# Performance work log

Measured on AMD Instinct MI355X. Metric: run time of the kernel, lower is better.

Reference implementation:

```python
import jax, jax.numpy as jnp
import numpy as np

D = 1024      # hidden_size
H = 16        # num_heads
HD = D // H   # head_dim = 64
FF = 4096     # intermediate_size
DEPTH = 2
S = 2048      # packed sequence length
NSEG = 4     # number of image segments
EPS = 1e-6


def setup_inputs() -> dict:
    key = jax.random.key(0)
    ks = jax.random.split(key, 8)
    hidden_states = jax.random.normal(ks[0], (S, D), jnp.float32)
    cu_seqlens = jnp.arange(NSEG + 1, dtype=jnp.int32) * (S // NSEG)
    # rotary embedding like RiceRotaryEmbedding(head_dim//2): freqs of dim HD//4
    # per spatial axis, h/w concatenated -> HD//2, then duplicated -> HD
    inv_freq = 1.0 / (10000.0 ** (jnp.arange(0, HD // 2, 2, dtype=jnp.float32) / (HD // 2)))
    pos = jnp.arange(S, dtype=jnp.float32)
    freqs = jnp.outer(pos, inv_freq)                       # [S, HD//4]
    emb = jnp.concatenate([freqs] * 4, axis=-1)            # [S, HD]
    cos, sin = jnp.cos(emb), jnp.sin(emb)

    def w(k, shape, fan):
        return jax.random.normal(k, shape, jnp.float32) / np.sqrt(fan)

    return {
        "hidden_states": hidden_states,
        "cu_seqlens": cu_seqlens,
        "cos": cos,
        "sin": sin,
        "ln1_g": jnp.ones((DEPTH, D), jnp.float32),
        "ln1_b": jnp.zeros((DEPTH, D), jnp.float32),
        "qkv_w": w(ks[1], (DEPTH, D, 3 * D), D),
        "qkv_b": jnp.zeros((DEPTH, 3 * D), jnp.float32),
        "proj_w": w(ks[2], (DEPTH, D, D), D),
        "proj_b": jnp.zeros((DEPTH, D), jnp.float32),
        "ln2_g": jnp.ones((DEPTH, D), jnp.float32),
        "ln2_b": jnp.zeros((DEPTH, D), jnp.float32),
        "fc1_w": w(ks[3], (DEPTH, D, FF), D),
        "fc1_b": jnp.zeros((DEPTH, FF), jnp.float32),
        "fc2_w": w(ks[4], (DEPTH, FF, D), FF),
        "fc2_b": jnp.zeros((DEPTH, D), jnp.float32),
    }


def _ln(x, g, b):
    m = jnp.mean(x, axis=-1, keepdims=True)
    v = jnp.mean(jnp.square(x - m), axis=-1, keepdims=True)
    return (x - m) / jnp.sqrt(v + EPS) * g + b


def _rotate_half(x):
    x1, x2 = jnp.split(x, 2, axis=-1)
    return jnp.concatenate([-x2, x1], axis=-1)


def reference(hidden_states, cu_seqlens, cos, sin,
              ln1_g, ln1_b, qkv_w, qkv_b, proj_w, proj_b,
              ln2_g, ln2_b, fc1_w, fc1_b, fc2_w, fc2_b):
    S_, D_ = hidden_states.shape
    # segment id per token from cu_seqlens -> block-diagonal additive mask
    seg = jnp.searchsorted(cu_seqlens[1:], jnp.arange(S_, dtype=jnp.int32), side="right")
    neg = jnp.finfo(jnp.float32).min
    bias = jnp.where(seg[:, None] == seg[None, :], 0.0, neg)   # [S, S]
    cos_e = cos[:, None, :]  # broadcast over heads, [S,1,HD]
    sin_e = sin[:, None, :]
    scale = 1.0 / np.sqrt(HD)

    x = hidden_states
    for i in range(DEPTH):
        # --- attention ---
        h = _ln(x, ln1_g[i], ln1_b[i])
        qkv = h @ qkv_w[i] + qkv_b[i]                           # [S, 3D]
        q, k, v = [t.reshape(S_, H, HD) for t in jnp.split(qkv, 3, axis=-1)]
        q = q * cos_e + _rotate_half(q) * sin_e
        k = k * cos_e + _rotate_half(k) * sin_e
        scores = jnp.einsum("shd,thd->hst", q, k) * scale + bias  # [H,S,S]
        w_ = jax.nn.softmax(scores.astype(jnp.float32), axis=-1)
        ao = jnp.einsum("hst,thd->shd", w_, v).reshape(S_, D_)
        x = x + ao @ proj_w[i] + proj_b[i]
        # --- mlp ---
        h2 = _ln(x, ln2_g[i], ln2_b[i])
        x = x + jax.nn.gelu(h2 @ fc1_w[i] + fc1_b[i], approximate=False) @ fc2_w[i] + fc2_b[i]
    return x
```

## Files before the change

### kernel.cpp

```cpp
#include <hip/hip_runtime.h>
#include <hip/hip_bf16.h>
#include <math.h>

#define Dm 1024
#define Hn 16
#define HDm 64
#define FFm 4096
#define Sn 2048
#define SEG 512
#define EPSV 1e-6f

typedef __attribute__((ext_vector_type(4))) float f32x4;
typedef __attribute__((ext_vector_type(8))) short s16x8;
typedef __attribute__((ext_vector_type(4))) short s16x4;

__device__ inline short f2bf(float f) {
  __hip_bfloat16 h = __float2bfloat16(f);
  short s;
  __builtin_memcpy(&s, &h, 2);
  return s;
}
__device__ inline float bf2f(short s) {
  unsigned u = ((unsigned)(unsigned short)s) << 16;
  float f;
  __builtin_memcpy(&f, &u, 4);
  return f;
}

__device__ inline float wred_sum(float v) {
#pragma unroll
  for (int m = 32; m > 0; m >>= 1) v += __shfl_xor(v, m, 64);
  return v;
}

__device__ inline void gld16(const short* g, short* lds_base) {
  __builtin_amdgcn_global_load_lds(
      (const __attribute__((address_space(1))) void*)g,
      (__attribute__((address_space(3))) void*)lds_base, 16, 0, 0);
}

__global__ __launch_bounds__(256) void ln_kernel(const float* __restrict__ x,
                                                 const float* __restrict__ g,
                                                 const float* __restrict__ b,
                                                 short* __restrict__ out) {
  const int row = blockIdx.x;
  const int tid = threadIdx.x;
  f32x4 v = *reinterpret_cast<const f32x4*>(x + (size_t)row * Dm + tid * 4);
  float s1 = v.x + v.y + v.z + v.w;
  float s2 = v.x * v.x + v.y * v.y + v.z * v.z + v.w * v.w;
  s1 = wred_sum(s1);
  s2 = wred_sum(s2);
  __shared__ float t1[4], t2[4];
  if ((tid & 63) == 0) { t1[tid >> 6] = s1; t2[tid >> 6] = s2; }
  __syncthreads();
  s1 = t1[0] + t1[1] + t1[2] + t1[3];
  s2 = t2[0] + t2[1] + t2[2] + t2[3];
  const float mean = s1 * (1.0f / Dm);
  const float var = s2 * (1.0f / Dm) - mean * mean;
  const float rstd = rsqrtf(var + EPSV);
  f32x4 gv = *reinterpret_cast<const f32x4*>(g + tid * 4);
  f32x4 bv = *reinterpret_cast<const f32x4*>(b + tid * 4);
  s16x4 o;
#pragma unroll
  for (int j = 0; j < 4; ++j)
    o[j] = f2bf((v[j] - mean) * rstd * gv[j] + bv[j]);
  *reinterpret_cast<s16x4*>(out + (size_t)row * Dm + tid * 4) = o;
}

template <int SPLIT>
__global__ __launch_bounds__(256) void redln_bf(const short* __restrict__ pb,
                                                const float* __restrict__ bias,
                                                const float* __restrict__ res,
                                                const float* __restrict__ g,
                                                const float* __restrict__ b,
                                                float* __restrict__ xout,
                                                short* __restrict__ h) {
  const int row = blockIdx.x;
  const int tid = threadIdx.x;
  const size_t idx = (size_t)row * Dm + tid * 4;
  f32x4 o = *reinterpret_cast<const f32x4*>(res + idx);
  o += *reinterpret_cast<const f32x4*>(bias + tid * 4);
#pragma unroll
  for (int s = 0; s < SPLIT; ++s) {
    s16x4 v = *reinterpret_cast<const s16x4*>(pb + (size_t)s * Sn * Dm + idx);
#pragma unroll
    for (int j = 0; j < 4; ++j) o[j] += bf2f(v[j]);
  }
  *reinterpret_cast<f32x4*>(xout + idx) = o;
  float s1 = o.x + o.y + o.z + o.w;
  float s2 = o.x * o.x + o.y * o.y + o.z * o.z + o.w * o.w;
  s1 = wred_sum(s1);
  s2 = wred_sum(s2);
  __shared__ float t1[4], t2[4];
  if ((tid & 63) == 0) { t1[tid >> 6] = s1; t2[tid >> 6] = s2; }
  __syncthreads();
  s1 = t1[0] + t1[1] + t1[2] + t1[3];
  s2 = t2[0] + t2[1] + t2[2] + t2[3];
  const float mean = s1 * (1.0f / Dm);
  const float var = s2 * (1.0f / Dm) - mean * mean;
  const float rstd = rsqrtf(var + EPSV);
  f32x4 gv = *reinterpret_cast<const f32x4*>(g + tid * 4);
  f32x4 bv = *reinterpret_cast<const f32x4*>(b + tid * 4);
  s16x4 ho;
#pragma unroll
  for (int j = 0; j < 4; ++j)
    ho[j] = f2bf((o[j] - mean) * rstd * gv[j] + bv[j]);
  *reinterpret_cast<s16x4*>(h + idx) = ho;
}

template <int SPLIT>
__global__ __launch_bounds__(256) void fcred_bf(const short* __restrict__ pb,
                                                const float* __restrict__ bias,
                                                const float* __restrict__ res,
                                                float* __restrict__ out) {
  const size_t i = ((size_t)blockIdx.x * 256 + threadIdx.x) * 4;
  f32x4 o = *reinterpret_cast<const f32x4*>(res + i);
  o += *reinterpret_cast<const f32x4*>(bias + (i & (Dm - 1)));
#pragma unroll
  for (int s = 0; s < SPLIT; ++s) {
    s16x4 v = *reinterpret_cast<const s16x4*>(pb + (size_t)s * Sn * Dm + i);
#pragma unroll
    for (int j = 0; j < 4; ++j) o[j] += bf2f(v[j]);
  }
  *reinterpret_cast<f32x4*>(out + i) = o;
}

struct WtJobs {
  const float* src[8];
  short* dst[8];
  int K[8], N[8], start[9];
};
__global__ __launch_bounds__(256) void wtall_kernel(WtJobs jb) {
  __shared__ float t[32][33];
  const int bid = blockIdx.x;
  int j = 0;
#pragma unroll
  for (int q = 1; q < 8; ++q)
    if (bid >= jb.start[q]) j = q;
  const int local = bid - jb.start[j];
  const int K = jb.K[j], N = jb.N[j];
  const int nx = N >> 5;
  const int n0 = (local % nx) * 32, k0 = (local / nx) * 32;
  const float* W = jb.src[j];
  short* Wt = jb.dst[j];
  const int tx = threadIdx.x & 31, ty = threadIdx.x >> 5;
#pragma unroll
  for (int r = 0; r < 32; r += 8)
    t[r + ty][tx] = W[(size_t)(k0 + r + ty) * N + n0 + tx];
  __syncthreads();
#pragma unroll
  for (int r = 0; r < 32; r += 8)
    Wt[(size_t)(n0 + r + ty) * K + k0 + tx] = f2bf(t[tx][r + ty]);
}

__global__ __launch_bounds__(256) void wtb_kernel(const short* __restrict__ V,
                                                  short* __restrict__ Vt,
                                                  int K, int N, int ldv) {
  __shared__ short t[32][34];
  const int n0 = blockIdx.x * 32, k0 = blockIdx.y * 32;
  const int tx = threadIdx.x & 31, ty = threadIdx.x >> 5;
#pragma unroll
  for (int r = 0; r < 32; r += 8)
    t[r + ty][tx] = V[(size_t)(k0 + r + ty) * ldv + n0 + tx];
  __syncthreads();
#pragma unroll
  for (int r = 0; r < 32; r += 8)
    Vt[(size_t)(n0 + r + ty) * K + k0 + tx] = t[tx][r + ty];
}

__global__ __launch_bounds__(256, 2) void attn2_kernel(const short* __restrict__ qkvb,
                                                       const short* __restrict__ vT,
                                                       short* __restrict__ ao) {
  __shared__ short Ks[512 * 64];
  const int tid = threadIdx.x;
  const int lane = tid & 63;
  const int wave = tid >> 6;
  const int l15 = lane & 15, lg = lane >> 4, rx = l15 & 7;
  const int qblk = blockIdx.x;
  const int z = blockIdx.y;
  const int seg = z & 3, head = z >> 2;
  const int qbase = seg * SEG + qblk * 64 + wave * 16;

  const int srow = tid >> 3;
  const int sch = ((tid & 7) ^ (srow & 7)) * 8;
  const short* Kg = qkvb + (size_t)(seg * SEG + srow) * 3072 + Dm +
                    head * HDm + sch;
#pragma unroll
  for (int j = 0; j < 16; ++j)
    gld16(Kg + (size_t)(j * 32) * 3072, &Ks[(j * 32 + wave * 8) * 64]);

  const short* Qg = qkvb + (size_t)(qbase + l15) * 3072 + head * HDm + lg * 8;
  s16x8 qf0 = *reinterpret_cast<const s16x8*>(Qg);
  s16x8 qf1 = *reinterpret_cast<const s16x8*>(Qg + 32);

  asm volatile("s_waitcnt vmcnt(0)" ::: "memory");
  __builtin_amdgcn_s_barrier();
  __builtin_amdgcn_sched_barrier(0);

  f32x4 acc[8][4] = {};
  __builtin_amdgcn_s_setprio(1);
#pragma unroll
  for (int kt = 0; kt < 8; ++kt) {
#pragma unroll
    for (int fj = 0; fj < 4; ++fj) {
      const int R = kt * 64 + fj * 16 + l15;
      s16x8 b0 = *reinterpret_cast<const s16x8*>(
          &Ks[R * 64 + ((lg ^ rx) << 3)]);
      s16x8 b1 = *reinterpret_cast<const s16x8*>(
          &Ks[R * 64 + (((lg + 4) ^ rx) << 3)]);
      acc[kt][fj] = __builtin_amdgcn_mfma_f32_16x16x32_bf16(qf0, b0, acc[kt][fj], 0, 0, 0);
      acc[kt][fj] = __builtin_amdgcn_mfma_f32_16x16x32_bf16(qf1, b1, acc[kt][fj], 0, 0, 0);
    }
  }
  __builtin_amdgcn_s_setprio(0);

  float mx[4], inv[4];
#pragma unroll
  for (int r = 0; r < 4; ++r) {
    float m = acc[0][0][r];
#pragma unroll
    for (int kt = 0; kt < 8; ++kt)
#pragma unroll
      for (int fj = 0; fj < 4; ++fj) m = fmaxf(m, acc[kt][fj][r]);
#pragma unroll
    for (int d = 1; d < 16; d <<= 1) m = fmaxf(m, __shfl_xor(m, d, 64));
    mx[r] = m * 0.125f;
  }
#pragma unroll
  for (int r = 0; r < 4; ++r) {
    float s = 0.f;
#pragma unroll
    for (int kt = 0; kt < 8; ++kt)
#pragma unroll
      for (int fj = 0; fj < 4; ++fj) {
        float pv = __expf(acc[kt][fj][r] * 0.125f - mx[r]);
        acc[kt][fj][r] = pv;
        s += pv;
      }
#pragma unroll
    for (int d = 1; d < 16; d <<= 1) s += __shfl_xor(s, d, 64);
    inv[r] = 1.0f / s;
  }

  __syncthreads();

  short* Psw = Ks + wave * 16 * 512;
#pragma unroll
  for (int kt = 0; kt < 8; ++kt)
#pragma unroll
    for (int fj = 0; fj < 4; ++fj)
#pragma unroll
      for (int r = 0; r < 4; ++r) {
        const int q = lg * 4 + r;
        const int k = kt * 64 + fj * 16 + l15;
        const int c = k >> 3;
        const int cs = (c & ~7) | ((c & 7) ^ (q & 7));
        Psw[q * 512 + cs * 8 + (k & 7)] = f2bf(acc[kt][fj][r]);
      }
  asm volatile("s_waitcnt lgkmcnt(0)" ::: "memory");
  __builtin_amdgcn_sched_barrier(0);

  f32x4 pv[4] = {};
  const short* Vg = vT + (size_t)(head * HDm) * Sn + seg * SEG;
  __builtin_amdgcn_s_setprio(1);
#pragma unroll
  for (int ks = 0; ks < 16; ++ks) {
    const int ca = ks * 4 + lg;
    const int csa = (ca & ~7) | ((ca & 7) ^ rx);
    s16x8 pa = *reinterpret_cast<const s16x8*>(&Psw[l15 * 512 + csa * 8]);
#pragma unroll
    for (int fj = 0; fj < 4; ++fj) {
      s16x8 pb = *reinterpret_cast<const s16x8*>(
          Vg + (size_t)(fj * 16 + l15) * Sn + ks * 32 + lg * 8);
      pv[fj] = __builtin_amdgcn_mfma_f32_16x16x32_bf16(pa, pb, pv[fj], 0, 0, 0);
    }
  }
  __builtin_amdgcn_s_setprio(0);

#pragma unroll
  for (int fj = 0; fj < 4; ++fj)
#pragma unroll
    for (int r = 0; r < 4; ++r)
      ao[(size_t)(qbase + lg * 4 + r) * Dm + head * HDm + fj * 16 + l15] =
          f2bf(pv[fj][r] * inv[r]);
}

struct GemmArgs {
  const short* A; int lda;
  const short* B; int ldb;
  void* C; int ldc;
  int M, N, K;
  const float* bias;
  const float* cosb; const float* sinb;
  float scale;
};

template <int BM, int BN, int SPLIT, int MODE>
__global__ __launch_bounds__(256) void gemm6(GemmArgs p) {
  constexpr int WN = 2;
  constexpr int WM = 2;
  constexpr int FI = BM / WM / 16;
  constexpr int FJ = BN / WN / 16;
  const int z = blockIdx.z;
  const short* A = p.A;
  const short* B = p.B;
  char* Cb = (char*)p.C;
  int kbase = 0, nkt = p.K >> 6;
  const int gx = gridDim.x;
  const int nwg = gx * gridDim.y;
  const int orig = blockIdx.y * gx + blockIdx.x;
  const int sid = (orig & 7) * (nwg >> 3) + (orig >> 3);
  const int tileM = (sid / gx) * BM;
  const int tileN = (sid % gx) * BN;
  if (MODE == 6) {
    kbase = z * (p.K / SPLIT);
    nkt = (p.K / SPLIT) >> 6;
    Cb += (size_t)z * p.M * p.N * 2;
  }
  __shared__ short As[BM * 64];
  __shared__ short Bs[BN * 64];
  const int tid = threadIdx.x;
  const int lane = tid & 63;
  const int wave = tid >> 6;
  const int l15 = lane & 15;
  const int lg = lane >> 4;
  const int rx = l15 & 7;
  const int wr = (wave / WN) * (BM / WM);
  const int wc = (wave % WN) * (BN / WN);
  const int srow = lane >> 3;
  const int scol = ((lane & 7) ^ srow) * 8;

  f32x4 acc[FI][FJ] = {};

  const short* Ag = A + (size_t)(tileM + wave * 8 + srow) * p.lda + scol + kbase;
  const short* Bg = B + (size_t)(tileN + wave * 8 + srow) * p.ldb + scol + kbase;

  for (int kt = 0; kt < nkt; ++kt) {
    const int k0 = kt * 64;
#pragma unroll
    for (int j = 0; j < BM / 32; ++j)
      gld16(Ag + (size_t)(j * 32) * p.lda + k0, &As[(j * 32 + wave * 8) * 64]);
#pragma unroll
    for (int j = 0; j < BN / 32; ++j)
      gld16(Bg + (size_t)(j * 32) * p.ldb + k0, &Bs[(j * 32 + wave * 8) * 64]);
    __syncthreads();
#pragma unroll
    for (int kk = 0; kk < 64; kk += 32) {
      const int kkc = kk >> 3;
      s16x8 af[FI], bfr[FJ];
#pragma unroll
      for (int f = 0; f < FI; ++f)
        af[f] = *reinterpret_cast<const s16x8*>(
            &As[(wr + f * 16 + l15) * 64 + (((lg + kkc) ^ rx) << 3)]);
#pragma unroll
      for (int f = 0; f < FJ; ++f)
        bfr[f] = *reinterpret_cast<const s16x8*>(
            &Bs[(wc + f * 16 + l15) * 64 + (((lg + kkc) ^ rx) << 3)]);
#pragma unroll
      for (int fi = 0; fi < FI; ++fi)
#pragma unroll
        for (int fj = 0; fj < FJ; ++fj)
          acc[fi][fj] = __builtin_amdgcn_mfma_f32_16x16x32_bf16(
              af[fi], bfr[fj], acc[fi][fj], 0, 0, 0);
    }
    __syncthreads();
  }

  if (MODE == 4) {
    short* Cs = (short*)Cb;
    const bool isqk = (tileN + wc) < 2048;
#pragma unroll
    for (int fi = 0; fi < FI; ++fi) {
#pragma unroll
      for (int fj = 0; fj < FJ; ++fj) {
#pragma unroll
        for (int r = 0; r < 4; ++r) {
          const int row = tileM + wr + fi * 16 + lg * 4 + r;
          const int col = tileN + wc + fj * 16 + l15;
          float a0 = acc[fi][fj][r] + p.bias[col];
          float vout;
          if (isqk) {
            float a1 = acc[fi][fj ^ 2][r] + p.bias[col ^ 32];
            const int dl = fj * 16 + l15;
            const float c = p.cosb[(size_t)row * HDm + dl];
            const float sn = p.sinb[(size_t)row * HDm + dl];
            vout = (fj < 2) ? (a0 * c - a1 * sn) : (a0 * c + a1 * sn);
          } else {
            vout = a0;
          }
          Cs[(size_t)row * p.ldc + col] = f2bf(vout);
        }
      }
    }
    return;
  }

#pragma unroll
  for (int fi = 0; fi < FI; ++fi) {
#pragma unroll
    for (int fj = 0; fj < FJ; ++fj) {
#pragma unroll
      for (int r = 0; r < 4; ++r) {
        const int row = tileM + wr + fi * 16 + lg * 4 + r;
        const int col = tileN + wc + fj * 16 + l15;
        float v = acc[fi][fj][r];
        if (MODE == 5) {
          v += p.bias[col];
          v = 0.5f * v * (1.0f + erff(v * 0.70710678118654752f));
        }
        reinterpret_cast<short*>(Cb)[(size_t)row * p.ldc + col] = f2bf(v);
      }
    }
  }
}

extern "C" void kernel_launch(void* const* d_in, const int* in_sizes, int n_in,
                              void* d_out, int out_size, void* d_ws, size_t ws_size,
                              hipStream_t stream) {
  const float* x0 = (const float*)d_in[0];
  const float* cosb = (const float*)d_in[2];
  const float* sinb = (const float*)d_in[3];
  const float* ln1_g = (const float*)d_in[4];
  const float* ln1_b = (const float*)d_in[5];
  const float* qkv_w = (const float*)d_in[6];
  const float* qkv_b = (const float*)d_in[7];
  const float* proj_w = (const float*)d_in[8];
  const float* proj_b = (const float*)d_in[9];
  const float* ln2_g = (const float*)d_in[10];
  const float* ln2_b = (const float*)d_in[11];
  const float* fc1_w = (const float*)d_in[12];
  const float* fc1_b = (const float*)d_in[13];
  const float* fc2_w = (const float*)d_in[14];
  const float* fc2_b = (const float*)d_in[15];

  char* ws = (char*)d_ws;
  size_t off = 0;
  auto alloc = [&](size_t bytes) {
    void* p = ws + off;
    off += (bytes + 255) & ~(size_t)255;
    return p;
  };
  short* wqkvT = (short*)alloc((size_t)2 * 3072 * 1024 * 2);
  short* wprojT = (short*)alloc((size_t)2 * 1024 * 1024 * 2);
  short* wfc1T = (short*)alloc((size_t)2 * 4096 * 1024 * 2);
  short* wfc2T = (short*)alloc((size_t)2 * 1024 * 4096 * 2);
  float* xbuf = (float*)alloc((size_t)Sn * Dm * 4);
  short* hbuf = (short*)alloc((size_t)Sn * Dm * 2);
  short* qkvb = (short*)alloc((size_t)Sn * 3 * Dm * 2);
  float* pbuf = (float*)alloc((size_t)4 * Sn * Dm * 4);
  short* pbufS = (short*)pbuf;
  short* ao = (short*)alloc((size_t)Sn * Dm * 2);
  short* ffn = (short*)alloc((size_t)Sn * FFm * 2);
  short* vT = ffn;
  (void)ws_size; (void)in_sizes; (void)n_in; (void)out_size;

  {
    WtJobs jb;
    int acc = 0;
    for (int i = 0; i < 2; ++i) {
      const int base = i * 4;
      jb.src[base + 0] = qkv_w + (size_t)i * Dm * 3072;
      jb.dst[base + 0] = wqkvT + (size_t)i * 3072 * Dm;
      jb.K[base + 0] = Dm; jb.N[base + 0] = 3072;
      jb.src[base + 1] = proj_w + (size_t)i * Dm * Dm;
      jb.dst[base + 1] = wprojT + (size_t)i * Dm * Dm;
      jb.K[base + 1] = Dm; jb.N[base + 1] = Dm;
      jb.src[base + 2] = fc1_w + (size_t)i * Dm * FFm;
      jb.dst[base + 2] = wfc1T + (size_t)i * FFm * Dm;
      jb.K[base + 2] = Dm; jb.N[base + 2] = FFm;
      jb.src[base + 3] = fc2_w + (size_t)i * FFm * Dm;
      jb.dst[base + 3] = wfc2T + (size_t)i * Dm * FFm;
      jb.K[base + 3] = FFm; jb.N[base + 3] = Dm;
    }
    for (int j = 0; j < 8; ++j) {
      jb.start[j] = acc;
      acc += (jb.N[j] >> 5) * (jb.K[j] >> 5);
    }
    jb.start[8] = acc;
    wtall_kernel<<<dim3(acc), 256, 0, stream>>>(jb);
  }

  ln_kernel<<<dim3(Sn), 256, 0, stream>>>(x0, ln1_g, ln1_b, hbuf);

  for (int i = 0; i < 2; ++i) {
    const float* xin = i ? (const float*)xbuf : x0;

    {
      GemmArgs p = {};
      p.A = hbuf; p.lda = Dm;
      p.B = wqkvT + (size_t)i * 3072 * Dm; p.ldb = Dm;
      p.C = qkvb; p.ldc = 3 * Dm;
      p.M = Sn; p.N = 3 * Dm; p.K = Dm;
      p.bias = qkv_b + i * 3 * Dm; p.cosb = cosb; p.sinb = sinb;
      gemm6<64, 128, 1, 4><<<dim3(24, 32, 1), 256, 0, stream>>>(p);
    }

    wtb_kernel<<<dim3(32, 64), 256, 0, stream>>>(qkvb + 2 * Dm, vT, Sn, Dm, 3 * Dm);

    attn2_kernel<<<dim3(8, 64), 256, 0, stream>>>(qkvb, vT, ao);

    {
      GemmArgs p = {};
      p.A = ao; p.lda = Dm;
      p.B = wprojT + (size_t)i * Dm * Dm; p.ldb = Dm;
      p.C = pbufS; p.ldc = Dm;
      p.M = Sn; p.N = Dm; p.K = Dm;
      gemm6<64, 64, 2, 6><<<dim3(16, 32, 2), 256, 0, stream>>>(p);
    }
    redln_bf<2><<<dim3(Sn), 256, 0, stream>>>(
        pbufS, proj_b + i * Dm, xin, ln2_g + i * Dm, ln2_b + i * Dm, xbuf, hbuf);

    {
      GemmArgs p = {};
      p.A = hbuf; p.lda = Dm;
      p.B = wfc1T + (size_t)i * FFm * Dm; p.ldb = Dm;
      p.C = ffn; p.ldc = FFm;
      p.M = Sn; p.N = FFm; p.K = Dm;
      p.bias = fc1_b + i * FFm;
      gemm6<64, 128, 1, 5><<<dim3(32, 32, 1), 256, 0, stream>>>(p);
    }

    {
      GemmArgs p = {};
      p.A = ffn; p.lda = FFm;
      p.B = wfc2T + (size_t)i * Dm * FFm; p.ldb = FFm;
      p.C = pbufS; p.ldc = Dm;
      p.M = Sn; p.N = Dm; p.K = FFm;
      gemm6<64, 128, 4, 6><<<dim3(8, 32, 4), 256, 0, stream>>>(p);
    }
    if (i == 0) {
      redln_bf<4><<<dim3(Sn), 256, 0, stream>>>(
          pbufS, fc2_b, xbuf, ln1_g + Dm, ln1_b + Dm, xbuf, hbuf);
    } else {
      fcred_bf<4><<<dim3(Sn * Dm / 1024), 256, 0, stream>>>(
          pbufS, fc2_b + Dm, xbuf, (float*)d_out);
    }
  }
}
```

Before: 297.4 us.

## Restructure attention kernel with 128-query blocks and V staged in LDS

The attention kernel now runs 512-thread blocks that each cover 128 queries. K and V^T are loaded into swizzled shared memory through asynchronous copies, so P·V reads V from LDS instead of global memory, and the K/V load cost is shared across twice as many queries. The P matrix is written to LDS and consumed in two halves of 256 keys so it fits in the freed K buffer. This uses 128KB of LDS per block, which limits occupancy, and the grid is flattened with head and segment as the fast index.

```diff
diff --git a/kernel.cpp b/kernel.cpp
--- a/kernel.cpp
+++ b/kernel.cpp
@@ -168,60 +168,68 @@
     Vt[(size_t)(n0 + r + ty) * K + k0 + tx] = t[tx][r + ty];
 }
 
-__global__ __launch_bounds__(256, 2) void attn2_kernel(const short* __restrict__ qkvb,
-                                                       const short* __restrict__ vT,
-                                                       short* __restrict__ ao) {
+__global__ __launch_bounds__(512, 2) void qksoftpv_kernel(const short* __restrict__ qkvb,
+                                                          const short* __restrict__ vT,
+                                                          short* __restrict__ ao) {
   __shared__ short Ks[512 * 64];
+  __shared__ short Vs[64 * 512];
   const int tid = threadIdx.x;
   const int lane = tid & 63;
   const int wave = tid >> 6;
   const int l15 = lane & 15, lg = lane >> 4, rx = l15 & 7;
-  const int qblk = blockIdx.x;
-  const int z = blockIdx.y;
+  const int qblk = blockIdx.x >> 6;
+  const int z = blockIdx.x & 63;
   const int seg = z & 3, head = z >> 2;
-  const int qbase = seg * SEG + qblk * 64 + wave * 16;
 
   const int srow = tid >> 3;
   const int sch = ((tid & 7) ^ (srow & 7)) * 8;
+
+  const short* Qg = qkvb +
+      (size_t)(seg * SEG + qblk * 128 + wave * 16 + l15) * 3072 + head * HDm +
+      lg * 8;
+  s16x8 qf0 = *reinterpret_cast<const s16x8*>(Qg);
+  s16x8 qf1 = *reinterpret_cast<const s16x8*>(Qg + 32);
+  __builtin_amdgcn_sched_barrier(0);
   const short* Kg = qkvb + (size_t)(seg * SEG + srow) * 3072 + Dm +
                     head * HDm + sch;
 #pragma unroll
-  for (int j = 0; j < 16; ++j)
-    gld16(Kg + (size_t)(j * 32) * 3072, &Ks[(j * 32 + wave * 8) * 64]);
-
-  const short* Qg = qkvb + (size_t)(qbase + l15) * 3072 + head * HDm + lg * 8;
-  s16x8 qf0 = *reinterpret_cast<const s16x8*>(Qg);
-  s16x8 qf1 = *reinterpret_cast<const s16x8*>(Qg + 32);
-
-  asm volatile("s_waitcnt vmcnt(0)" ::: "memory");
+  for (int j = 0; j < 8; ++j)
+    gld16(Kg + (size_t)(j * 64) * 3072, &Ks[(j * 64 + wave * 8) * 64]);
+  __builtin_amdgcn_sched_barrier(0);
+  {
+    const short* Vg = vT + (size_t)(head * 64) * Sn + seg * SEG;
+#pragma unroll
+    for (int j = 0; j < 8; ++j) {
+      const int d = j * 8 + wave;
+      const int c = (lane & ~7) | ((lane & 7) ^ (d & 7));
+      gld16(Vg + (size_t)d * Sn + c * 8, &Vs[d * 512]);
+    }
+  }
+  asm volatile("s_waitcnt vmcnt(8)" ::: "memory");
   __builtin_amdgcn_s_barrier();
   __builtin_amdgcn_sched_barrier(0);
 
-  f32x4 acc[8][4] = {};
+  f32x4 acc[32];
+#pragma unroll
+  for (int j = 0; j < 32; ++j) acc[j] = f32x4{0.f, 0.f, 0.f, 0.f};
   __builtin_amdgcn_s_setprio(1);
 #pragma unroll
-  for (int kt = 0; kt < 8; ++kt) {
-#pragma unroll
-    for (int fj = 0; fj < 4; ++fj) {
-      const int R = kt * 64 + fj * 16 + l15;
-      s16x8 b0 = *reinterpret_cast<const s16x8*>(
-          &Ks[R * 64 + ((lg ^ rx) << 3)]);
-      s16x8 b1 = *reinterpret_cast<const s16x8*>(
-          &Ks[R * 64 + (((lg + 4) ^ rx) << 3)]);
-      acc[kt][fj] = __builtin_amdgcn_mfma_f32_16x16x32_bf16(qf0, b0, acc[kt][fj], 0, 0, 0);
-      acc[kt][fj] = __builtin_amdgcn_mfma_f32_16x16x32_bf16(qf1, b1, acc[kt][fj], 0, 0, 0);
-    }
+  for (int j = 0; j < 32; ++j) {
+    const int R = j * 16 + l15;
+    s16x8 b0 = *reinterpret_cast<const s16x8*>(&Ks[R * 64 + ((lg ^ rx) << 3)]);
+    s16x8 b1 = *reinterpret_cast<const s16x8*>(
+        &Ks[R * 64 + (((lg + 4) ^ rx) << 3)]);
+    acc[j] = __builtin_amdgcn_mfma_f32_16x16x32_bf16(qf0, b0, acc[j], 0, 0, 0);
+    acc[j] = __builtin_amdgcn_mfma_f32_16x16x32_bf16(qf1, b1, acc[j], 0, 0, 0);
   }
   __builtin_amdgcn_s_setprio(0);
 
   float mx[4], inv[4];
 #pragma unroll
   for (int r = 0; r < 4; ++r) {
-    float m = acc[0][0][r];
-#pragma unroll
-    for (int kt = 0; kt < 8; ++kt)
-#pragma unroll
-      for (int fj = 0; fj < 4; ++fj) m = fmaxf(m, acc[kt][fj][r]);
+    float m = acc[0][r];
+#pragma unroll
+    for (int j = 1; j < 32; ++j) m = fmaxf(m, acc[j][r]);
 #pragma unroll
     for (int d = 1; d < 16; d <<= 1) m = fmaxf(m, __shfl_xor(m, d, 64));
     mx[r] = m * 0.125f;
@@ -230,59 +238,70 @@
   for (int r = 0; r < 4; ++r) {
     float s = 0.f;
 #pragma unroll
-    for (int kt = 0; kt < 8; ++kt)
-#pragma unroll
-      for (int fj = 0; fj < 4; ++fj) {
-        float pv = __expf(acc[kt][fj][r] * 0.125f - mx[r]);
-        acc[kt][fj][r] = pv;
-        s += pv;
-      }
+    for (int j = 0; j < 32; ++j) {
+      float pv = __expf(acc[j][r] * 0.125f - mx[r]);
+      acc[j][r] = pv;
+      s += pv;
+    }
 #pragma unroll
     for (int d = 1; d < 16; d <<= 1) s += __shfl_xor(s, d, 64);
     inv[r] = 1.0f / s;
   }
 
   __syncthreads();
-
-  short* Psw = Ks + wave * 16 * 512;
-#pragma unroll
-  for (int kt = 0; kt < 8; ++kt)
+  asm volatile("s_waitcnt vmcnt(0)" ::: "memory");
+
+  short* Ps = Ks;
+  f32x4 pv[4] = {};
+  const int q2 = wave * 16 + l15;
+  const int sxr = (q2 ^ (q2 >> 3)) & 7;
+#pragma unroll
+  for (int kh = 0; kh < 2; ++kh) {
+#pragma unroll
+    for (int jj = 0; jj < 16; ++jj) {
+      const int j = kh * 16 + jj;
+#pragma unroll
+      for (int r = 0; r < 4; ++r) {
+        const int q = wave * 16 + lg * 4 + r;
+        const int kp = jj * 16 + l15;
+        const int c = kp >> 3;
+        const int sxw = (q ^ (q >> 3)) & 7;
+        const int cs = (c & 24) | ((c & 7) ^ sxw);
+        Ps[q * 256 + cs * 8 + (kp & 7)] = f2bf(acc[j][r]);
+      }
+    }
+    asm volatile("s_waitcnt lgkmcnt(0)" ::: "memory");
+    __builtin_amdgcn_sched_barrier(0);
+    __builtin_amdgcn_s_setprio(1);
+#pragma unroll
+    for (int ks = 0; ks < 8; ++ks) {
+      const int ca = ks * 4 + lg;
+      const int csa = (ca & 24) | ((ca & 7) ^ sxr);
+      s16x8 pa = *reinterpret_cast<const s16x8*>(&Ps[q2 * 256 + csa * 8]);
+#pragma unroll
+      for (int fj = 0; fj < 4; ++fj) {
+        const int d = fj * 16 + l15;
+        const int cb = kh * 32 + ks * 4 + lg;
+        const int csb = (cb & ~7) | ((cb & 7) ^ (d & 7));
+        s16x8 pb = *reinterpret_cast<const s16x8*>(&Vs[d * 512 + csb * 8]);
+        pv[fj] = __builtin_amdgcn_mfma_f32_16x16x32_bf16(pa, pb, pv[fj], 0, 0, 0);
+      }
+    }
+    __builtin_amdgcn_s_setprio(0);
+    asm volatile("s_waitcnt lgkmcnt(0)" ::: "memory");
+    __builtin_amdgcn_sched_barrier(0);
+  }
+
+#pragma unroll
+  for (int r = 0; r < 4; ++r) {
+    const float iv = inv[r];
+    const size_t rowg =
+        (size_t)(seg * SEG + qblk * 128 + wave * 16 + lg * 4 + r) * Dm +
+        head * 64;
 #pragma unroll
     for (int fj = 0; fj < 4; ++fj)
-#pragma unroll
-      for (int r = 0; r < 4; ++r) {
-        const int q = lg * 4 + r;
-        const int k = kt * 64 + fj * 16 + l15;
-        const int c = k >> 3;
-        const int cs = (c & ~7) | ((c & 7) ^ (q & 7));
-        Psw[q * 512 + cs * 8 + (k & 7)] = f2bf(acc[kt][fj][r]);
-      }
-  asm volatile("s_waitcnt lgkmcnt(0)" ::: "memory");
-  __builtin_amdgcn_sched_barrier(0);
-
-  f32x4 pv[4] = {};
-  const short* Vg = vT + (size_t)(head * HDm) * Sn + seg * SEG;
-  __builtin_amdgcn_s_setprio(1);
-#pragma unroll
-  for (int ks = 0; ks < 16; ++ks) {
-    const int ca = ks * 4 + lg;
-    const int csa = (ca & ~7) | ((ca & 7) ^ rx);
-    s16x8 pa = *reinterpret_cast<const s16x8*>(&Psw[l15 * 512 + csa * 8]);
-#pragma unroll
-    for (int fj = 0; fj < 4; ++fj) {
-      s16x8 pb = *reinterpret_cast<const s16x8*>(
-          Vg + (size_t)(fj * 16 + l15) * Sn + ks * 32 + lg * 8);
-      pv[fj] = __builtin_amdgcn_mfma_f32_16x16x32_bf16(pa, pb, pv[fj], 0, 0, 0);
-    }
-  }
-  __builtin_amdgcn_s_setprio(0);
-
-#pragma unroll
-  for (int fj = 0; fj < 4; ++fj)
-#pragma unroll
-    for (int r = 0; r < 4; ++r)
-      ao[(size_t)(qbase + lg * 4 + r) * Dm + head * HDm + fj * 16 + l15] =
-          f2bf(pv[fj][r] * inv[r]);
+      ao[rowg + fj * 16 + l15] = f2bf(pv[fj][r] * iv);
+  }
 }
 
 struct GemmArgs {
@@ -497,7 +516,7 @@
 
     wtb_kernel<<<dim3(32, 64), 256, 0, stream>>>(qkvb + 2 * Dm, vT, Sn, Dm, 3 * Dm);
 
-    attn2_kernel<<<dim3(8, 64), 256, 0, stream>>>(qkvb, vT, ao);
+    qksoftpv_kernel<<<dim3(256), 512, 0, stream>>>(qkvb, vT, ao);
 
     {
       GemmArgs p = {};
```

Result: faster. 272.3 us, median of 2 (-8.4%).
